# Kernel optimization log

Hardware: AMD Instinct MI355X
Metric: run time of the kernel (lower is better)

## Reference

```python
import jax, jax.numpy as jnp
import numpy as np

N_RAYS = 65536
N_SAMPLES = 96


def setup_inputs() -> dict:
    key = jax.random.key(0)
    k1, k2, k3 = jax.random.split(key, 3)
    rgb = jax.random.uniform(k1, (N_RAYS, N_SAMPLES, 3), dtype=jnp.float32)
    # SDF values near the surface, small magnitude
    sdf = jax.random.normal(k2, (N_RAYS, N_SAMPLES), dtype=jnp.float32) * 0.1
    # monotonically increasing sample depths along each ray
    z_vals = jnp.sort(
        jax.random.uniform(k3, (N_RAYS, N_SAMPLES), dtype=jnp.float32,
                           minval=0.1, maxval=5.0), axis=-1)
    return {"rgb": rgb, "sdf": sdf, "z_vals": z_vals, "beta": 10}


def reference(rgb, sdf, z_vals, beta):
    # sdf2alpha: alpha = 1 - exp(-beta * sigmoid(-sdf * beta))
    alpha = 1.0 - jnp.exp(-beta * jax.nn.sigmoid(-sdf * beta))  # [N, S]
    # exclusive cumprod of (1 - alpha + 1e-10): transmittance
    trans = jnp.cumprod(
        jnp.concatenate([jnp.ones_like(alpha[:, :1]), 1.0 - alpha + 1e-10],
                        axis=-1), axis=-1)[:, :-1]  # [N, S]
    weights = alpha * trans  # [N, S]
    rendered_rgb = jnp.sum(weights[..., None] * rgb, axis=-2)  # [N, 3]
    rendered_depth = jnp.sum(weights * z_vals, axis=-1)  # [N]
    return (rendered_depth, rendered_rgb, sdf, z_vals)
```

## Files before the change

### kernel.cpp

```cpp
#include <hip/hip_runtime.h>


#define SDFR_NS 96

struct f3 { float x, y, z; };

__global__ __launch_bounds__(256, 8) void sdf_render_kernel(
    const float* __restrict__ rgb,
    const float* __restrict__ sdf,
    const float* __restrict__ z_vals,
    const int*   __restrict__ beta_p,
    float* __restrict__ out_depth,
    float* __restrict__ out_rgb,
    float* __restrict__ out_sdf,
    float* __restrict__ out_z,
    int n_rays)
{
    const int tid = blockIdx.x * 256 + threadIdx.x;
    const int ray = tid >> 5;
    const int l   = tid & 31;
    if (ray >= n_rays) return;

    const long sb = (long)ray * SDFR_NS + 3 * l;
    const long rb = (long)ray * (SDFR_NS * 3) + 9 * l;

    const f3 sv = *(const f3*)(sdf    + sb);
    const f3 zv = *(const f3*)(z_vals + sb);
    const f3 ca = *(const f3*)(rgb + rb + 0);
    const f3 cb = *(const f3*)(rgb + rb + 3);
    const f3 cc = *(const f3*)(rgb + rb + 6);
    __builtin_amdgcn_sched_barrier(0);

    int bi = *beta_p;
    float beta;
    if (bi > 1000000 || bi < -1000000) {
        union { int i; float f; } u; u.i = bi; beta = u.f;
    } else {
        beta = (float)bi;
    }

    const float e0 = __expf(-beta * __builtin_amdgcn_rcpf(1.0f + __expf(sv.x * beta)));
    const float e1 = __expf(-beta * __builtin_amdgcn_rcpf(1.0f + __expf(sv.y * beta)));
    const float e2 = __expf(-beta * __builtin_amdgcn_rcpf(1.0f + __expf(sv.z * beta)));
    const float a0 = 1.0f - e0, t0 = e0 + 1e-10f;
    const float a1 = 1.0f - e1, t1 = e1 + 1e-10f;
    const float a2 = 1.0f - e2, t2 = e2 + 1e-10f;

    *(f3*)(out_sdf + sb) = sv;
    *(f3*)(out_z   + sb) = zv;

    const float m = t0 * t1 * t2;
    float scan = m;
    #pragma unroll
    for (int d = 1; d < 32; d <<= 1) {
        float v = __shfl_up(scan, d, 32);
        if (l >= d) scan *= v;
    }
    float E = __shfl_up(scan, 1, 32);
    if (l == 0) E = 1.0f;

    const float w0 = a0 * E;
    const float w1 = a1 * E * t0;
    const float w2 = a2 * E * t0 * t1;

    float depth = w0 * zv.x + w1 * zv.y + w2 * zv.z;
    float r0    = w0 * ca.x + w1 * cb.x + w2 * cc.x;
    float r1    = w0 * ca.y + w1 * cb.y + w2 * cc.y;
    float r2    = w0 * ca.z + w1 * cb.z + w2 * cc.z;

    #pragma unroll
    for (int d = 16; d >= 1; d >>= 1) {
        depth += __shfl_xor(depth, d, 32);
        r0    += __shfl_xor(r0, d, 32);
        r1    += __shfl_xor(r1, d, 32);
        r2    += __shfl_xor(r2, d, 32);
    }

    if (l == 0) {
        out_depth[ray] = depth;
        f3 o; o.x = r0; o.y = r1; o.z = r2;
        *(f3*)(out_rgb + (long)ray * 3) = o;
    }
}

extern "C" void kernel_launch(void* const* d_in, const int* in_sizes, int n_in,
                              void* d_out, int out_size, void* d_ws, size_t ws_size,
                              hipStream_t stream) {
    (void)n_in; (void)d_ws; (void)ws_size; (void)out_size;

    const float* rgb    = (const float*)d_in[0];
    const float* sdf    = (const float*)d_in[1];
    const float* z      = (const float*)d_in[2];
    const int*   beta_p = (const int*)d_in[3];

    const int n_rays = in_sizes[1] / SDFR_NS;

    float* out_depth = (float*)d_out;
    float* out_rgb   = out_depth + n_rays;
    float* out_sdf   = out_rgb   + (size_t)n_rays * 3;
    float* out_z     = out_sdf   + (size_t)n_rays * SDFR_NS;

    const long total_threads = (long)n_rays * 32;
    const int  grid = (int)((total_threads + 255) / 256);
    sdf_render_kernel<<<grid, 256, 0, stream>>>(
        rgb, sdf, z, beta_p, out_depth, out_rgb, out_sdf, out_z, n_rays);
}
```

Before: 170.8 us.

## Process four rays per warp-group with double-buffered software-pipelined loads

Each 32-lane group now handles four rays per block instead of one. Loads for the next ray are issued before computing the current one, using two register buffers and sched barriers so memory latency overlaps the math. Index arithmetic also switches from long to int. This cuts the grid size by four and adds more registers per thread, which could lower occupancy.

```diff
diff --git a/kernel.cpp b/kernel.cpp
--- a/kernel.cpp
+++ b/kernel.cpp
@@ -2,42 +2,21 @@
 
 
 #define SDFR_NS 96
+#define SDFR_RPP 8
+#define SDFR_PASSES 4
+#define SDFR_RPB (SDFR_RPP * SDFR_PASSES)
 
 struct f3 { float x, y, z; };
 
-__global__ __launch_bounds__(256, 8) void sdf_render_kernel(
-    const float* __restrict__ rgb,
-    const float* __restrict__ sdf,
-    const float* __restrict__ z_vals,
-    const int*   __restrict__ beta_p,
-    float* __restrict__ out_depth,
-    float* __restrict__ out_rgb,
-    float* __restrict__ out_sdf,
-    float* __restrict__ out_z,
-    int n_rays)
+__device__ __forceinline__ void render_ray(
+    int ray, int l, float beta,
+    const f3& sv, const f3& zv, const f3& ca, const f3& cb, const f3& cc,
+    int sb,
+    float* __restrict__ out_depth, float* __restrict__ out_rgb,
+    float* __restrict__ out_sdf,   float* __restrict__ out_z)
 {
-    const int tid = blockIdx.x * 256 + threadIdx.x;
-    const int ray = tid >> 5;
-    const int l   = tid & 31;
-    if (ray >= n_rays) return;
-
-    const long sb = (long)ray * SDFR_NS + 3 * l;
-    const long rb = (long)ray * (SDFR_NS * 3) + 9 * l;
-
-    const f3 sv = *(const f3*)(sdf    + sb);
-    const f3 zv = *(const f3*)(z_vals + sb);
-    const f3 ca = *(const f3*)(rgb + rb + 0);
-    const f3 cb = *(const f3*)(rgb + rb + 3);
-    const f3 cc = *(const f3*)(rgb + rb + 6);
-    __builtin_amdgcn_sched_barrier(0);
-
-    int bi = *beta_p;
-    float beta;
-    if (bi > 1000000 || bi < -1000000) {
-        union { int i; float f; } u; u.i = bi; beta = u.f;
-    } else {
-        beta = (float)bi;
-    }
+    *(f3*)(out_sdf + sb) = sv;
+    *(f3*)(out_z   + sb) = zv;
 
     const float e0 = __expf(-beta * __builtin_amdgcn_rcpf(1.0f + __expf(sv.x * beta)));
     const float e1 = __expf(-beta * __builtin_amdgcn_rcpf(1.0f + __expf(sv.y * beta)));
@@ -45,9 +24,6 @@
     const float a0 = 1.0f - e0, t0 = e0 + 1e-10f;
     const float a1 = 1.0f - e1, t1 = e1 + 1e-10f;
     const float a2 = 1.0f - e2, t2 = e2 + 1e-10f;
-
-    *(f3*)(out_sdf + sb) = sv;
-    *(f3*)(out_z   + sb) = zv;
 
     const float m = t0 * t1 * t2;
     float scan = m;
@@ -79,8 +55,78 @@
     if (l == 0) {
         out_depth[ray] = depth;
         f3 o; o.x = r0; o.y = r1; o.z = r2;
-        *(f3*)(out_rgb + (long)ray * 3) = o;
+        *(f3*)(out_rgb + ray * 3) = o;
     }
+}
+
+__global__ __launch_bounds__(256, 8) void sdf_render_kernel(
+    const float* __restrict__ rgb,
+    const float* __restrict__ sdf,
+    const float* __restrict__ z_vals,
+    const int*   __restrict__ beta_p,
+    float* __restrict__ out_depth,
+    float* __restrict__ out_rgb,
+    float* __restrict__ out_sdf,
+    float* __restrict__ out_z,
+    int n_rays)
+{
+    const int t = threadIdx.x;
+    const int g = t >> 5;
+    const int l = t & 31;
+
+    int bi = *beta_p;
+    float beta;
+    if (bi > 1000000 || bi < -1000000) {
+        union { int i; float f; } u; u.i = bi; beta = u.f;
+    } else {
+        beta = (float)bi;
+    }
+
+    const int rA0 = blockIdx.x * SDFR_RPB + 0 * SDFR_RPP + g;
+    const int rB0 = blockIdx.x * SDFR_RPB + 1 * SDFR_RPP + g;
+    const int rA1 = blockIdx.x * SDFR_RPB + 2 * SDFR_RPP + g;
+    const int rB1 = blockIdx.x * SDFR_RPB + 3 * SDFR_RPP + g;
+
+    f3 svA, zvA, caA, cbA, ccA; int sbA;
+    f3 svB, zvB, caB, cbB, ccB; int sbB;
+
+#define SDFR_LOAD(SFX, RAY)                                         \
+    do {                                                            \
+        sb##SFX = (RAY) * SDFR_NS + 3 * l;                          \
+        const int rb_ = (RAY) * (SDFR_NS * 3) + 9 * l;              \
+        sv##SFX = *(const f3*)(sdf    + sb##SFX);                   \
+        zv##SFX = *(const f3*)(z_vals + sb##SFX);                   \
+        ca##SFX = *(const f3*)(rgb + rb_ + 0);                      \
+        cb##SFX = *(const f3*)(rgb + rb_ + 3);                      \
+        cc##SFX = *(const f3*)(rgb + rb_ + 6);                      \
+    } while (0)
+
+#define SDFR_RUN(SFX, RAY)                                          \
+    render_ray((RAY), l, beta, sv##SFX, zv##SFX, ca##SFX, cb##SFX,  \
+               cc##SFX, sb##SFX, out_depth, out_rgb, out_sdf, out_z)
+
+    const bool vA0 = (rA0 < n_rays);
+    const bool vB0 = (rB0 < n_rays);
+    const bool vA1 = (rA1 < n_rays);
+    const bool vB1 = (rB1 < n_rays);
+
+    if (vA0) SDFR_LOAD(A, rA0);
+    if (vB0) SDFR_LOAD(B, rB0);
+    __builtin_amdgcn_sched_barrier(0);
+
+    if (vA0) SDFR_RUN(A, rA0);
+    if (vA1) SDFR_LOAD(A, rA1);
+    __builtin_amdgcn_sched_barrier(0);
+
+    if (vB0) SDFR_RUN(B, rB0);
+    if (vB1) SDFR_LOAD(B, rB1);
+    __builtin_amdgcn_sched_barrier(0);
+
+    if (vA1) SDFR_RUN(A, rA1);
+    if (vB1) SDFR_RUN(B, rB1);
+
+#undef SDFR_LOAD
+#undef SDFR_RUN
 }
 
 extern "C" void kernel_launch(void* const* d_in, const int* in_sizes, int n_in,
@@ -100,8 +146,7 @@
     float* out_sdf   = out_rgb   + (size_t)n_rays * 3;
     float* out_z     = out_sdf   + (size_t)n_rays * SDFR_NS;
 
-    const long total_threads = (long)n_rays * 32;
-    const int  grid = (int)((total_threads + 255) / 256);
+    const int grid = (n_rays + SDFR_RPB - 1) / SDFR_RPB;
     sdf_render_kernel<<<grid, 256, 0, stream>>>(
         rgb, sdf, z, beta_p, out_depth, out_rgb, out_sdf, out_z, n_rays);
 }
```

New measurement: 176.4 us. 3.3% more time.

## Split sdf/z passthrough copy into dedicated vectorized nontemporal copy blocks

Applied to the files above, without the earlier changes.

Moves the copy of sdf and z_vals to the outputs out of the compute threads and into 2048 dedicated blocks at the front of the grid. These blocks run a grid-stride loop with 16-byte vector loads and nontemporal stores. Compute threads now only load and reduce. Index math also changes from 64-bit to 32-bit. The risk is that the copy blocks re-read sdf and z from memory (or cache) that the compute blocks also read, and the grid split changes how work is scheduled.

```diff
diff --git a/kernel.cpp b/kernel.cpp
--- a/kernel.cpp
+++ b/kernel.cpp
@@ -2,8 +2,10 @@
 
 
 #define SDFR_NS 96
+#define SDFR_NCOPY 2048
 
 struct f3 { float x, y, z; };
+typedef float fv4 __attribute__((ext_vector_type(4)));
 
 __global__ __launch_bounds__(256, 8) void sdf_render_kernel(
     const float* __restrict__ rgb,
@@ -16,13 +18,33 @@
     float* __restrict__ out_z,
     int n_rays)
 {
-    const int tid = blockIdx.x * 256 + threadIdx.x;
-    const int ray = tid >> 5;
-    const int l   = tid & 31;
+    const int t = threadIdx.x;
+
+    if (blockIdx.x < SDFR_NCOPY) {
+        const int n4 = (n_rays * SDFR_NS) / 4;
+        const int stride = SDFR_NCOPY * 256;
+        const fv4* __restrict__ s4 = (const fv4*)sdf;
+        const fv4* __restrict__ z4 = (const fv4*)z_vals;
+        fv4* __restrict__ os4 = (fv4*)out_sdf;
+        fv4* __restrict__ oz4 = (fv4*)out_z;
+
+        for (int i = blockIdx.x * 256 + t; i < n4; i += stride) {
+            const fv4 a = s4[i];
+            const fv4 b = z4[i];
+            __builtin_nontemporal_store(a, os4 + i);
+            __builtin_nontemporal_store(b, oz4 + i);
+        }
+        return;
+    }
+
+    const int cbid = blockIdx.x - SDFR_NCOPY;
+    const int tid  = cbid * 256 + t;
+    const int ray  = tid >> 5;
+    const int l    = tid & 31;
     if (ray >= n_rays) return;
 
-    const long sb = (long)ray * SDFR_NS + 3 * l;
-    const long rb = (long)ray * (SDFR_NS * 3) + 9 * l;
+    const int sb = ray * SDFR_NS + 3 * l;
+    const int rb = ray * (SDFR_NS * 3) + 9 * l;
 
     const f3 sv = *(const f3*)(sdf    + sb);
     const f3 zv = *(const f3*)(z_vals + sb);
@@ -45,9 +67,6 @@
     const float a0 = 1.0f - e0, t0 = e0 + 1e-10f;
     const float a1 = 1.0f - e1, t1 = e1 + 1e-10f;
     const float a2 = 1.0f - e2, t2 = e2 + 1e-10f;
-
-    *(f3*)(out_sdf + sb) = sv;
-    *(f3*)(out_z   + sb) = zv;
 
     const float m = t0 * t1 * t2;
     float scan = m;
@@ -79,7 +98,7 @@
     if (l == 0) {
         out_depth[ray] = depth;
         f3 o; o.x = r0; o.y = r1; o.z = r2;
-        *(f3*)(out_rgb + (long)ray * 3) = o;
+        *(f3*)(out_rgb + ray * 3) = o;
     }
 }
 
@@ -100,8 +119,8 @@
     float* out_sdf   = out_rgb   + (size_t)n_rays * 3;
     float* out_z     = out_sdf   + (size_t)n_rays * SDFR_NS;
 
-    const long total_threads = (long)n_rays * 32;
-    const int  grid = (int)((total_threads + 255) / 256);
+    const int comp_blocks = (n_rays * 32 + 255) / 256;
+    const int grid = SDFR_NCOPY + comp_blocks;
     sdf_render_kernel<<<grid, 256, 0, stream>>>(
         rgb, sdf, z, beta_p, out_depth, out_rgb, out_sdf, out_z, n_rays);
 }
```

New measurement: 164.7 us. 3.6% less time.
